# Kernel tuning notes

Hardware: AMD Instinct MI355X
Metric: run time of the kernel (lower is better)

The kernel has to match this reference:

```python
import jax, jax.numpy as jnp
import numpy as np

SEQ_LEN = 2048
EMBED = 1024
HIDDEN = 1024
BATCH = 8

def setup_inputs() -> dict:
    key = jax.random.key(0)
    ks = jax.random.split(key, 7)
    scale = (6.0 / (EMBED + HIDDEN)) ** 0.5  # xavier_uniform
    inputs = jax.random.normal(ks[0], (BATCH, SEQ_LEN, EMBED), dtype=jnp.float32)
    Wq = jax.random.uniform(ks[1], (EMBED, HIDDEN), minval=-scale, maxval=scale, dtype=jnp.float32)
    Wk = jax.random.uniform(ks[2], (EMBED, HIDDEN), minval=-scale, maxval=scale, dtype=jnp.float32)
    Wv = jax.random.uniform(ks[3], (EMBED, HIDDEN), minval=-scale, maxval=scale, dtype=jnp.float32)
    bq = jax.random.normal(ks[4], (HIDDEN,), dtype=jnp.float32) * 0.01
    bk = jax.random.normal(ks[5], (HIDDEN,), dtype=jnp.float32) * 0.01
    bv = jax.random.normal(ks[6], (HIDDEN,), dtype=jnp.float32) * 0.01
    return {"inputs": inputs, "Wq": Wq, "bq": bq, "Wk": Wk, "bk": bk, "Wv": Wv, "bv": bv}

def reference(inputs, Wq, bq, Wk, bk, Wv, bv):
    # inputs: [B, S, E]
    q = jnp.einsum('bse,eh->bsh', inputs, Wq) + bq  # [B,S,H]
    k = jnp.einsum('bse,eh->bsh', inputs, Wk) + bk
    v = jnp.einsum('bse,eh->bsh', inputs, Wv) + bv
    scores = jnp.einsum('bqh,bkh->bqk', q, k) / jnp.sqrt(jnp.float32(HIDDEN))  # [B,S,S]
    causal = jnp.tril(jnp.ones((SEQ_LEN, SEQ_LEN), dtype=bool))
    scores = jnp.where(causal, scores, -jnp.inf)
    attn = jax.nn.softmax(scores, axis=-1)
    return jnp.einsum('bqk,bkh->bqh', attn, v)
```

## Files before the change

kernel.cpp:

```cpp
#include <hip/hip_runtime.h>

#define B_ 8
#define S_ 2048
#define E_ 1024
#define H_ 1024

typedef __attribute__((ext_vector_type(8))) short bf16x8;
typedef __attribute__((ext_vector_type(4))) float f32x4;

__device__ inline short f2bf(float f) {
  unsigned u = __builtin_bit_cast(unsigned, f);
  unsigned r = u + 0x7FFFu + ((u >> 16) & 1u);
  return (short)(r >> 16);
}
__device__ inline float bf2f(short s) {
  unsigned u = ((unsigned)(unsigned short)s) << 16;
  return __builtin_bit_cast(float, u);
}

__device__ inline void async16(const void* g, void* l) {
  __builtin_amdgcn_global_load_lds((const __attribute__((address_space(1))) void*)g,
                                   (__attribute__((address_space(3))) void*)l,
                                   16, 0, 0);
}

__global__ __launch_bounds__(256)
void prep(const float* __restrict__ X, short* __restrict__ Xbf,
          const float* __restrict__ W0, const float* __restrict__ W1,
          const float* __restrict__ W2, short* __restrict__ Wt) {
  __shared__ __align__(16) float t[64][65];
  const int bid = blockIdx.x;
  if (bid < 2048) {
    const int n4 = (int)((size_t)B_ * S_ * E_ / 4);
    const int stride = 2048 * 256;
    for (int i = bid * 256 + threadIdx.x; i < n4; i += stride) {
      float4 v = ((const float4*)X)[i];
      short4 o;
      o.x = f2bf(v.x); o.y = f2bf(v.y); o.z = f2bf(v.z); o.w = f2bf(v.w);
      ((short4*)Xbf)[i] = o;
    }
    return;
  }
  const int idx = bid - 2048;
  const int zz = idx >> 8;
  const int rem = idx & 255;
  const float* W = (zz == 0) ? W0 : (zz == 1) ? W1 : W2;
  short* out = Wt + (size_t)zz * H_ * E_;
  const int h0 = (rem & 15) * 64, e0 = (rem >> 4) * 64;
  const int r = threadIdx.x >> 4;
  const int c = (threadIdx.x & 15) * 4;
#pragma unroll
  for (int p = 0; p < 4; ++p) {
    int rr = r + p * 16;
    float4 v = *(const float4*)&W[(size_t)(e0 + rr) * H_ + h0 + c];
    t[rr][c + 0] = v.x; t[rr][c + 1] = v.y; t[rr][c + 2] = v.z; t[rr][c + 3] = v.w;
  }
  __syncthreads();
#pragma unroll
  for (int p = 0; p < 4; ++p) {
    int rr = r + p * 16;
    short4 o;
    o.x = f2bf(t[c + 0][rr]); o.y = f2bf(t[c + 1][rr]);
    o.z = f2bf(t[c + 2][rr]); o.w = f2bf(t[c + 3][rr]);
    *(short4*)&out[(size_t)(h0 + rr) * E_ + e0 + c] = o;
  }
}


#define BAR() asm volatile("s_barrier" ::: "memory")
#define VMC(n) asm volatile("s_waitcnt vmcnt(" #n ")" ::: "memory")

#define RD_B(buf, ks)                                                        \
  _Pragma("unroll")                                                          \
  for (int n = 0; n < 4; ++n)                                                \
    bfr[n] = *(const bf16x8*)(lBp + (buf) * 32768 + (ks) * 16384 +           \
                              ((wc * 64 + n * 16 + lr) << 6) + aCol)

#define RD_A(buf, ks, mh)                                                    \
  _Pragma("unroll")                                                          \
  for (int m = 0; m < 4; ++m)                                                \
    af[m] = *(const bf16x8*)(lAp + (buf) * 32768 + (ks) * 16384 +            \
                             ((wr * 128 + (mh) * 64 + m * 16 + lr) << 6) + aCol)

#define MFMA16(mh)                                                           \
  _Pragma("unroll")                                                          \
  for (int m = 0; m < 4; ++m) {                                              \
    _Pragma("unroll")                                                        \
    for (int n = 0; n < 4; ++n)                                              \
      acc[(mh) * 4 + m][n] = __builtin_amdgcn_mfma_f32_16x16x32_bf16(        \
          af[m], bfr[n], acc[(mh) * 4 + m][n], 0, 0, 0);                     \
  }

#define STAGE_A(buf, ks, kt) do {                                            \
    const short* _s = A + (size_t)(m0 + srow) * ldA + (kt) * 64 + (ks) * 32 + scol; \
    char* _d = (char*)lAp + (buf) * 32768 + (ks) * 16384 + wv * 1024;        \
    async16(_s, _d);                                                         \
    async16(_s + (size_t)128 * ldA, _d + 8192);                              \
  } while (0)

#define STAGE_B(buf, ks, kt) do {                                            \
    const short* _s = Bt + (size_t)(n0 + srow) * ldBt + (kt) * 64 + (ks) * 32 + scol; \
    char* _d = (char*)lBp + (buf) * 32768 + (ks) * 16384 + wv * 1024;        \
    async16(_s, _d);                                                         \
    async16(_s + (size_t)128 * ldBt, _d + 8192);                             \
  } while (0)

#define PHASE(buf, ks, mh, STG, WT) do {                                     \
    if ((mh) == 0) { RD_B(buf, ks); }                                        \
    RD_A(buf, ks, mh);                                                       \
    STG;                                                                     \
    WT;                                                                      \
    BAR();                                                                   \
    asm volatile("s_waitcnt lgkmcnt(0)" ::: "memory");                       \
    __builtin_amdgcn_sched_barrier(0);                                       \
    __builtin_amdgcn_s_setprio(1);                                           \
    MFMA16(mh);                                                              \
    __builtin_amdgcn_s_setprio(0);                                           \
    BAR();                                                                   \
  } while (0)

template <int MODE>
__global__ __launch_bounds__(512, 2)
void gemm8(const short* __restrict__ A, const short* __restrict__ Bt,
           void* __restrict__ C0, void* __restrict__ C1, void* __restrict__ C2,
           const float* __restrict__ b0, const float* __restrict__ b1,
           const float* __restrict__ b2,
           float* __restrict__ PlO,
           int K, int ldA, int ldBt, int ldC,
           size_t zsA, size_t zsB, size_t zsC, float scale) {
  int bx, by, z;
  {
    const int bid = blockIdx.x;
    if (MODE == 0) {
      int t = (bid & 7) * 96 + (bid >> 3);
      by = t / 12; bx = t % 12; z = 0;
    } else if (MODE == 1) {
      int t = (bid & 7) * 36 + (bid >> 3);
      z = t / 36;
      int u = t % 36;
      by = 0;
      while (u >= (by + 1) * (by + 2) / 2) ++by;
      bx = u - by * (by + 1) / 2;
    } else {
      int t = (bid & 7) * 32 + (bid >> 3);
      z = t >> 5;
      int rem = t & 31;
      by = rem >> 2; bx = rem & 3;
    }
  }
  A  += (size_t)z * zsA;
  Bt += (size_t)z * zsB;

  __shared__ __align__(16) short lA[2][2][256 * 32];
  __shared__ __align__(16) short lB[2][2][256 * 32];
  __shared__ float sLi[256];
  const char* lAp = (const char*)&lA[0][0][0];
  const char* lBp = (const char*)&lB[0][0][0];

  const int tid = threadIdx.x;
  const int lane = tid & 63;
  const int wv = tid >> 6;
  const int wr = wv >> 2, wc = wv & 3;
  const int lr = lane & 15, kg = lane >> 4;
  const int m0 = by * 256, n0 = bx * 256;
  const int kEnd = (MODE == 2) ? (by + 1) * 256 : K;
  const int nt = kEnd >> 6;
  const int nIter = nt >> 1;

  const int aCol = (kg * 16) ^ ((lr & 8) << 2);
  const int srow = tid >> 2;
  const int scol = (((tid & 3) * 16) ^ (tid & 32)) >> 1;

  if (MODE == 2 && tid < 256) {
    float l = 0.f;
    for (int kt = 0; kt <= by; ++kt)
      l += PlO[((size_t)z * 8 + kt) * S_ + m0 + tid];
    sLi[tid] = 1.f / l;
  }

  f32x4 acc[8][4];
#pragma unroll
  for (int m = 0; m < 8; ++m)
#pragma unroll
    for (int n = 0; n < 4; ++n) acc[m][n] = (f32x4){0.f, 0.f, 0.f, 0.f};
  bf16x8 bfr[4], af[4];

  STAGE_B(0, 0, 0); STAGE_A(0, 0, 0); STAGE_B(0, 1, 0); STAGE_A(0, 1, 0);
  STAGE_B(1, 0, 1); STAGE_A(1, 0, 1); STAGE_B(1, 1, 1);
  VMC(6);
  if (MODE == 2) asm volatile("s_waitcnt lgkmcnt(0)" ::: "memory");
  BAR();

  for (int i = 0; i < nIter; ++i) {
    const int T = 2 * i;
    const bool lastI = (i == nIter - 1);
    PHASE(0, 0, 0, STAGE_A(1, 1, T + 1), (void)0);
    PHASE(0, 0, 1, if (!lastI) { STAGE_B(0, 0, T + 2); }, (void)0);
    PHASE(0, 1, 0, if (!lastI) { STAGE_A(0, 0, T + 2); }, (void)0);
    PHASE(0, 1, 1, if (!lastI) { STAGE_B(0, 1, T + 2); },
          if (lastI) { VMC(0); } else { VMC(6); });
    PHASE(1, 0, 0, if (!lastI) { STAGE_A(0, 1, T + 2); }, (void)0);
    PHASE(1, 0, 1, if (!lastI) { STAGE_B(1, 0, T + 3); }, (void)0);
    PHASE(1, 1, 0, if (!lastI) { STAGE_A(1, 0, T + 3); }, (void)0);
    PHASE(1, 1, 1, if (!lastI) { STAGE_B(1, 1, T + 3); },
          if (!lastI) { VMC(6); });
  }

  if (MODE == 0 && (n0 >> 10) == 2) {
    short* tv = (short*)lAp;
    const int zb = by >> 3;
    const int sb = (by & 7) * 256;
    short* VT = (short*)C2 + (size_t)zb * H_ * S_;
    const int hseg = n0 - 2048;
#pragma unroll
    for (int p = 0; p < 2; ++p) {
      if ((wc >> 1) == p) {
#pragma unroll
        for (int mq = 0; mq < 8; ++mq) {
          int sr = wr * 128 + (mq >> 2) * 64 + (mq & 3) * 16 + kg * 4;
#pragma unroll
          for (int n = 0; n < 4; ++n) {
            int c = wc * 64 + n * 16 + lr;
            float bb = b2[hseg + c];
            f32x4 v = acc[mq][n];
            short4 o;
            o.x = f2bf(v[0] + bb); o.y = f2bf(v[1] + bb);
            o.z = f2bf(v[2] + bb); o.w = f2bf(v[3] + bb);
            *(short4*)&tv[(c & 127) * 264 + sr] = o;
          }
        }
      }
      __syncthreads();
#pragma unroll
      for (int i = 0; i < 8; ++i) {
        int chunk = i * 512 + tid;
        int h = chunk >> 5, sc = (chunk & 31) * 8;
        bf16x8 v8 = *(const bf16x8*)&tv[h * 264 + sc];
        *(bf16x8*)&VT[(size_t)(hseg + p * 128 + h) * S_ + sb + sc] = v8;
      }
      __syncthreads();
    }
    return;
  }
  if (MODE == 1) {
    float* tmpL = (float*)lAp;
    short* C = (short*)C0 + (size_t)z * zsC;
    const bool diag = (bx == by);
#pragma unroll
    for (int mq = 0; mq < 8; ++mq) {
      int rt0 = wr * 128 + (mq >> 2) * 64 + (mq & 3) * 16 + kg * 4;
#pragma unroll
      for (int r = 0; r < 4; ++r) {
        int rt = rt0 + r;
        float se = 0.f;
#pragma unroll
        for (int n = 0; n < 4; ++n) {
          int c = wc * 64 + n * 16 + lr;
          bool ok = !diag || (c <= rt);
          short sh = ok ? f2bf(__expf(acc[mq][n][r] * scale)) : (short)0;
          se += bf2f(sh);
          C[(size_t)(m0 + rt) * ldC + n0 + c] = sh;
        }
#pragma unroll
        for (int o = 1; o < 16; o <<= 1) se += __shfl_xor(se, o);
        if (lr == 0) tmpL[rt * 4 + wc] = se;
      }
    }
    __syncthreads();
    if (tid < 256) {
      float l = tmpL[tid * 4 + 0] + tmpL[tid * 4 + 1] +
                tmpL[tid * 4 + 2] + tmpL[tid * 4 + 3];
      PlO[((size_t)z * 8 + bx) * S_ + m0 + tid] = l;
    }
    return;
  }
#pragma unroll
  for (int mq = 0; mq < 8; ++mq) {
    int rowb = m0 + wr * 128 + (mq >> 2) * 64 + (mq & 3) * 16 + kg * 4;
#pragma unroll
    for (int n = 0; n < 4; ++n) {
      int col = n0 + wc * 64 + n * 16 + lr;
      f32x4 v = acc[mq][n];
      if (MODE == 0) {
        int seg = n0 >> 10;
        const float* bp = (seg == 0) ? b0 : b1;
        short* C = (short*)((seg == 0) ? C0 : C1);
        int cl = col & 1023;
        float bb = bp[cl];
#pragma unroll
        for (int r = 0; r < 4; ++r)
          C[(size_t)(rowb + r) * ldC + cl] = f2bf(v[r] + bb);
      } else {
        float* C = (float*)C0 + (size_t)z * zsC;
        f32x4 liv = *(const f32x4*)&sLi[rowb - m0];
#pragma unroll
        for (int r = 0; r < 4; ++r)
          C[(size_t)(rowb + r) * ldC + col] = v[r] * liv[r];
      }
    }
  }
}

extern "C" void kernel_launch(void* const* d_in, const int* in_sizes, int n_in,
                              void* d_out, int out_size, void* d_ws, size_t ws_size,
                              hipStream_t stream) {
  const float* X  = (const float*)d_in[0];
  const float* Wq = (const float*)d_in[1];
  const float* bq = (const float*)d_in[2];
  const float* Wk = (const float*)d_in[3];
  const float* bk = (const float*)d_in[4];
  const float* Wv = (const float*)d_in[5];
  const float* bv = (const float*)d_in[6];

  char* ws = (char*)d_ws;
  const size_t MB = 1024ull * 1024ull;
  short* Pbuf = (short*)ws;
  short* Xbf  = (short*)ws;
  short* Q    = (short*)(ws + 64 * MB);
  short* Kb   = (short*)(ws + 96 * MB);
  short* Vt   = (short*)(ws + 128 * MB);
  short* Wt   = (short*)(ws + 160 * MB);
  float* Pl   = (float*)(ws + 160 * MB);

  prep<<<2816, 256, 0, stream>>>(X, Xbf, Wq, Wk, Wv, Wt);
  gemm8<0><<<768, 512, 0, stream>>>(
      Xbf, Wt, Q, Kb, Vt, bq, bk, bv, nullptr,
      E_, E_, E_, H_, 0, 0, 0, 1.f);
  gemm8<1><<<288, 512, 0, stream>>>(
      Q, Kb, Pbuf, nullptr, nullptr, nullptr, nullptr, nullptr, Pl,
      H_, H_, H_, S_, (size_t)S_ * H_, (size_t)S_ * H_, (size_t)S_ * S_, 0.03125f);
  gemm8<2><<<256, 512, 0, stream>>>(
      Pbuf, Vt, d_out, nullptr, nullptr, nullptr, nullptr, nullptr, Pl,
      S_, S_, S_, H_, (size_t)S_ * S_, (size_t)H_ * S_, (size_t)S_ * H_, 1.f);
}
```

Baseline: 273.3 us.

## Use 128x256 tiles for attention GEMMs to balance causal work

Splits the QK^T and PV GEMMs into a new gemm4 kernel with 128-row tiles instead of 256, doubling block counts (576 and 512). The finer granularity is meant to reduce tail imbalance from the triangular causal workload and improve CU occupancy. It also reorders PV blocks so the longest rows (largest by) launch first. The cost is lower data reuse per tile, a rewritten staging pipeline with new vmcnt accounting, and a recomputed triangular block-index mapping.

```diff
diff --git a/kernel.cpp b/kernel.cpp
--- a/kernel.cpp
+++ b/kernel.cpp
@@ -66,7 +66,6 @@
   }
 }
 
-
 #define BAR() asm volatile("s_barrier" ::: "memory")
 #define VMC(n) asm volatile("s_waitcnt vmcnt(" #n ")" ::: "memory")
 
@@ -125,35 +124,16 @@
            void* __restrict__ C0, void* __restrict__ C1, void* __restrict__ C2,
            const float* __restrict__ b0, const float* __restrict__ b1,
            const float* __restrict__ b2,
-           float* __restrict__ PlO,
-           int K, int ldA, int ldBt, int ldC,
-           size_t zsA, size_t zsB, size_t zsC, float scale) {
-  int bx, by, z;
+           int K, int ldA, int ldBt, int ldC, float scale) {
+  int bx, by;
   {
     const int bid = blockIdx.x;
-    if (MODE == 0) {
-      int t = (bid & 7) * 96 + (bid >> 3);
-      by = t / 12; bx = t % 12; z = 0;
-    } else if (MODE == 1) {
-      int t = (bid & 7) * 36 + (bid >> 3);
-      z = t / 36;
-      int u = t % 36;
-      by = 0;
-      while (u >= (by + 1) * (by + 2) / 2) ++by;
-      bx = u - by * (by + 1) / 2;
-    } else {
-      int t = (bid & 7) * 32 + (bid >> 3);
-      z = t >> 5;
-      int rem = t & 31;
-      by = rem >> 2; bx = rem & 3;
-    }
-  }
-  A  += (size_t)z * zsA;
-  Bt += (size_t)z * zsB;
+    int t = (bid & 7) * 96 + (bid >> 3);
+    by = t / 12; bx = t % 12;
+  }
 
   __shared__ __align__(16) short lA[2][2][256 * 32];
   __shared__ __align__(16) short lB[2][2][256 * 32];
-  __shared__ float sLi[256];
   const char* lAp = (const char*)&lA[0][0][0];
   const char* lBp = (const char*)&lB[0][0][0];
 
@@ -163,21 +143,13 @@
   const int wr = wv >> 2, wc = wv & 3;
   const int lr = lane & 15, kg = lane >> 4;
   const int m0 = by * 256, n0 = bx * 256;
-  const int kEnd = (MODE == 2) ? (by + 1) * 256 : K;
-  const int nt = kEnd >> 6;
+  const int nt = K >> 6;
   const int nIter = nt >> 1;
 
   const int aCol = (kg * 16) ^ ((lr & 8) << 2);
   const int srow = tid >> 2;
   const int scol = (((tid & 3) * 16) ^ (tid & 32)) >> 1;
 
-  if (MODE == 2 && tid < 256) {
-    float l = 0.f;
-    for (int kt = 0; kt <= by; ++kt)
-      l += PlO[((size_t)z * 8 + kt) * S_ + m0 + tid];
-    sLi[tid] = 1.f / l;
-  }
-
   f32x4 acc[8][4];
 #pragma unroll
   for (int m = 0; m < 8; ++m)
@@ -188,7 +160,6 @@
   STAGE_B(0, 0, 0); STAGE_A(0, 0, 0); STAGE_B(0, 1, 0); STAGE_A(0, 1, 0);
   STAGE_B(1, 0, 1); STAGE_A(1, 0, 1); STAGE_B(1, 1, 1);
   VMC(6);
-  if (MODE == 2) asm volatile("s_waitcnt lgkmcnt(0)" ::: "memory");
   BAR();
 
   for (int i = 0; i < nIter; ++i) {
@@ -206,7 +177,7 @@
           if (!lastI) { VMC(6); });
   }
 
-  if (MODE == 0 && (n0 >> 10) == 2) {
+  if ((n0 >> 10) == 2) {
     short* tv = (short*)lAp;
     const int zb = by >> 3;
     const int sb = (by & 7) * 256;
@@ -242,13 +213,152 @@
     }
     return;
   }
+#pragma unroll
+  for (int mq = 0; mq < 8; ++mq) {
+    int rowb = m0 + wr * 128 + (mq >> 2) * 64 + (mq & 3) * 16 + kg * 4;
+#pragma unroll
+    for (int n = 0; n < 4; ++n) {
+      int col = n0 + wc * 64 + n * 16 + lr;
+      f32x4 v = acc[mq][n];
+      int seg = n0 >> 10;
+      const float* bp = (seg == 0) ? b0 : b1;
+      short* C = (short*)((seg == 0) ? C0 : C1);
+      int cl = col & 1023;
+      float bb = bp[cl];
+#pragma unroll
+      for (int r = 0; r < 4; ++r)
+        C[(size_t)(rowb + r) * ldC + cl] = f2bf(v[r] + bb);
+    }
+  }
+}
+
+
+#define RD_B4(buf, ks)                                                       \
+  _Pragma("unroll")                                                          \
+  for (int n = 0; n < 4; ++n)                                                \
+    bfr[n] = *(const bf16x8*)(lBp + (buf) * 32768 + (ks) * 16384 +           \
+                              ((wc * 64 + n * 16 + lr) << 6) + aCol)
+
+#define RD_A4(buf, ks)                                                       \
+  _Pragma("unroll")                                                          \
+  for (int m = 0; m < 4; ++m)                                                \
+    af[m] = *(const bf16x8*)(lAp + (buf) * 16384 + (ks) * 8192 +             \
+                             ((wr * 64 + m * 16 + lr) << 6) + aCol)
+
+#define MFMA16Q()                                                            \
+  _Pragma("unroll")                                                          \
+  for (int m = 0; m < 4; ++m) {                                              \
+    _Pragma("unroll")                                                        \
+    for (int n = 0; n < 4; ++n)                                              \
+      acc[m][n] = __builtin_amdgcn_mfma_f32_16x16x32_bf16(                   \
+          af[m], bfr[n], acc[m][n], 0, 0, 0);                                \
+  }
+
+#define STAGE_A4(buf, ks, kt) do {                                           \
+    const short* _s = A + (size_t)(m0 + srow) * ldA + (kt) * 64 + (ks) * 32 + scol; \
+    char* _d = (char*)lAp + (buf) * 16384 + (ks) * 8192 + wv * 1024;         \
+    async16(_s, _d);                                                         \
+  } while (0)
+
+#define STAGE_B4(buf, ks, kt) do {                                           \
+    const short* _s = Bt + (size_t)(n0 + srow) * ldBt + (kt) * 64 + (ks) * 32 + scol; \
+    char* _d = (char*)lBp + (buf) * 32768 + (ks) * 16384 + wv * 1024;        \
+    async16(_s, _d);                                                         \
+    async16(_s + (size_t)128 * ldBt, _d + 8192);                             \
+  } while (0)
+
+#define PHASE4(buf, ks, STG, WT) do {                                        \
+    RD_B4(buf, ks);                                                          \
+    RD_A4(buf, ks);                                                          \
+    STG;                                                                     \
+    WT;                                                                      \
+    BAR();                                                                   \
+    asm volatile("s_waitcnt lgkmcnt(0)" ::: "memory");                       \
+    __builtin_amdgcn_sched_barrier(0);                                       \
+    __builtin_amdgcn_s_setprio(1);                                           \
+    MFMA16Q();                                                               \
+    __builtin_amdgcn_s_setprio(0);                                           \
+    BAR();                                                                   \
+  } while (0)
+
+template <int MODE>
+__global__ __launch_bounds__(512, 2)
+void gemm4(const short* __restrict__ A, const short* __restrict__ Bt,
+           void* __restrict__ C0, float* __restrict__ PlO,
+           int K, int ldA, int ldBt, int ldC,
+           size_t zsA, size_t zsB, size_t zsC, float scale) {
+  const int z = blockIdx.x & 7;
+  const int rr0 = blockIdx.x >> 3;
+  int bx, by;
+  if (MODE == 1) {
+    by = 0; int ac = 0;
+    while (rr0 >= ac + (by >> 1) + 1) { ac += (by >> 1) + 1; ++by; }
+    bx = rr0 - ac;
+  } else {
+    by = 15 - (rr0 >> 2); bx = rr0 & 3;
+  }
+  A  += (size_t)z * zsA;
+  Bt += (size_t)z * zsB;
+
+  __shared__ __align__(16) short lA[2][2][128 * 32];
+  __shared__ __align__(16) short lB[2][2][256 * 32];
+  __shared__ float sLi[128];
+  const char* lAp = (const char*)&lA[0][0][0];
+  const char* lBp = (const char*)&lB[0][0][0];
+
+  const int tid = threadIdx.x;
+  const int lane = tid & 63;
+  const int wv = tid >> 6;
+  const int wr = wv >> 2, wc = wv & 3;
+  const int lr = lane & 15, kg = lane >> 4;
+  const int m0 = by * 128, n0 = bx * 256;
+  const int kEnd = (MODE == 2) ? ((by >> 1) + 1) * 256 : K;
+  const int nt = kEnd >> 6;
+  const int nIter = nt >> 1;
+
+  const int aCol = (kg * 16) ^ ((lr & 8) << 2);
+  const int srow = tid >> 2;
+  const int scol = (((tid & 3) * 16) ^ (tid & 32)) >> 1;
+
+  if (MODE == 2 && tid < 128) {
+    float l = 0.f;
+    for (int kt = 0; kt <= (by >> 1); ++kt)
+      l += PlO[((size_t)z * 8 + kt) * S_ + m0 + tid];
+    sLi[tid] = 1.f / l;
+  }
+
+  f32x4 acc[4][4];
+#pragma unroll
+  for (int m = 0; m < 4; ++m)
+#pragma unroll
+    for (int n = 0; n < 4; ++n) acc[m][n] = (f32x4){0.f, 0.f, 0.f, 0.f};
+  bf16x8 bfr[4], af[4];
+
+  STAGE_B4(0, 0, 0); STAGE_A4(0, 0, 0); STAGE_B4(0, 1, 0); STAGE_A4(0, 1, 0);
+  STAGE_B4(1, 0, 1); STAGE_A4(1, 0, 1);
+  VMC(3);
+  if (MODE == 2) asm volatile("s_waitcnt lgkmcnt(0)" ::: "memory");
+  BAR();
+
+  for (int i = 0; i < nIter; ++i) {
+    const int T = 2 * i;
+    const bool lastI = (i == nIter - 1);
+    PHASE4(0, 0, { STAGE_B4(1, 1, T + 1); STAGE_A4(1, 1, T + 1); }, (void)0);
+    PHASE4(0, 1, if (!lastI) { STAGE_B4(0, 0, T + 2); STAGE_A4(0, 0, T + 2); },
+           if (lastI) { VMC(3); } else { VMC(6); });
+    PHASE4(1, 0, if (!lastI) { STAGE_B4(0, 1, T + 2); STAGE_A4(0, 1, T + 2); },
+           if (lastI) { VMC(0); } else { VMC(6); });
+    PHASE4(1, 1, if (!lastI) { STAGE_B4(1, 0, T + 3); STAGE_A4(1, 0, T + 3); VMC(3); },
+           (void)0);
+  }
+
   if (MODE == 1) {
     float* tmpL = (float*)lAp;
     short* C = (short*)C0 + (size_t)z * zsC;
-    const bool diag = (bx == by);
-#pragma unroll
-    for (int mq = 0; mq < 8; ++mq) {
-      int rt0 = wr * 128 + (mq >> 2) * 64 + (mq & 3) * 16 + kg * 4;
+    const bool diag = (bx == (by >> 1));
+#pragma unroll
+    for (int m = 0; m < 4; ++m) {
+      int rt0 = wr * 64 + m * 16 + kg * 4;
 #pragma unroll
       for (int r = 0; r < 4; ++r) {
         int rt = rt0 + r;
@@ -256,8 +366,8 @@
 #pragma unroll
         for (int n = 0; n < 4; ++n) {
           int c = wc * 64 + n * 16 + lr;
-          bool ok = !diag || (c <= rt);
-          short sh = ok ? f2bf(__expf(acc[mq][n][r] * scale)) : (short)0;
+          bool ok = !diag || (n0 + c <= m0 + rt);
+          short sh = ok ? f2bf(__expf(acc[m][n][r] * scale)) : (short)0;
           se += bf2f(sh);
           C[(size_t)(m0 + rt) * ldC + n0 + c] = sh;
         }
@@ -267,32 +377,24 @@
       }
     }
     __syncthreads();
-    if (tid < 256) {
+    if (tid < 128) {
       float l = tmpL[tid * 4 + 0] + tmpL[tid * 4 + 1] +
                 tmpL[tid * 4 + 2] + tmpL[tid * 4 + 3];
       PlO[((size_t)z * 8 + bx) * S_ + m0 + tid] = l;
     }
     return;
   }
-#pragma unroll
-  for (int mq = 0; mq < 8; ++mq) {
-    int rowb = m0 + wr * 128 + (mq >> 2) * 64 + (mq & 3) * 16 + kg * 4;
-#pragma unroll
-    for (int n = 0; n < 4; ++n) {
-      int col = n0 + wc * 64 + n * 16 + lr;
-      f32x4 v = acc[mq][n];
-      if (MODE == 0) {
-        int seg = n0 >> 10;
-        const float* bp = (seg == 0) ? b0 : b1;
-        short* C = (short*)((seg == 0) ? C0 : C1);
-        int cl = col & 1023;
-        float bb = bp[cl];
-#pragma unroll
-        for (int r = 0; r < 4; ++r)
-          C[(size_t)(rowb + r) * ldC + cl] = f2bf(v[r] + bb);
-      } else {
-        float* C = (float*)C0 + (size_t)z * zsC;
-        f32x4 liv = *(const f32x4*)&sLi[rowb - m0];
+  {
+    float* C = (float*)C0 + (size_t)z * zsC;
+#pragma unroll
+    for (int m = 0; m < 4; ++m) {
+      int rl = wr * 64 + m * 16 + kg * 4;
+      f32x4 liv = *(const f32x4*)&sLi[rl];
+      int rowb = m0 + rl;
+#pragma unroll
+      for (int n = 0; n < 4; ++n) {
+        int col = n0 + wc * 64 + n * 16 + lr;
+        f32x4 v = acc[m][n];
 #pragma unroll
         for (int r = 0; r < 4; ++r)
           C[(size_t)(rowb + r) * ldC + col] = v[r] * liv[r];
@@ -324,12 +426,11 @@
 
   prep<<<2816, 256, 0, stream>>>(X, Xbf, Wq, Wk, Wv, Wt);
   gemm8<0><<<768, 512, 0, stream>>>(
-      Xbf, Wt, Q, Kb, Vt, bq, bk, bv, nullptr,
-      E_, E_, E_, H_, 0, 0, 0, 1.f);
-  gemm8<1><<<288, 512, 0, stream>>>(
-      Q, Kb, Pbuf, nullptr, nullptr, nullptr, nullptr, nullptr, Pl,
-      H_, H_, H_, S_, (size_t)S_ * H_, (size_t)S_ * H_, (size_t)S_ * S_, 0.03125f);
-  gemm8<2><<<256, 512, 0, stream>>>(
-      Pbuf, Vt, d_out, nullptr, nullptr, nullptr, nullptr, nullptr, Pl,
-      S_, S_, S_, H_, (size_t)S_ * S_, (size_t)H_ * S_, (size_t)S_ * H_, 1.f);
-}
+      Xbf, Wt, Q, Kb, Vt, bq, bk, bv, E_, E_, E_, H_, 1.f);
+  gemm4<1><<<576, 512, 0, stream>>>(
+      Q, Kb, Pbuf, Pl, H_, H_, H_, S_,
+      (size_t)S_ * H_, (size_t)S_ * H_, (size_t)S_ * S_, 0.03125f);
+  gemm4<2><<<512, 512, 0, stream>>>(
+      Pbuf, Vt, d_out, Pl, S_, S_, S_, H_,
+      (size_t)S_ * S_, (size_t)H_ * S_, (size_t)S_ * H_, 1.f);
+}
```

Result: faster. 261.1 us (-4.5%).
